# Optimization experiments

Hardware: AMD Instinct MI355X
Metric: run time of the kernel (lower is better)

## Reference

```python
import jax, jax.numpy as jnp
import numpy as np
import math

B, L = 512, 32768
NUM_C, NUM_D = 16, 8
RECIPTIVE, STRIDES = 512, 256
EPS = 1e-4


def setup_inputs() -> dict:
    key = jax.random.key(0)
    kx, kw = jax.random.split(key)
    x = jax.random.normal(kx, (B, L), dtype=jnp.float32)
    stdv = 1.0 / math.sqrt(RECIPTIVE)
    weight = jax.random.uniform(kw, (NUM_C, NUM_D, RECIPTIVE), dtype=jnp.float32,
                                minval=-stdv, maxval=stdv)
    return {"x": x, "weight": weight}


def reference(x, weight):
    # x: [B, L], weight: [C, D, R]
    Lx = x.shape[1]
    # sigma = (W W^T + eps I)^{-1} per capsule, [C, D, D]
    wc = jnp.einsum('cdr,cer->cde', weight, weight)
    sigma = jnp.linalg.inv(wc + EPS * jnp.eye(NUM_D, dtype=weight.dtype))
    # circular sliding windows: [W, R] index map (wraparound matches torch.cat branch)
    starts = jnp.arange(0, Lx, STRIDES)
    idx = (starts[:, None] + jnp.arange(RECIPTIVE)[None, :]) % Lx
    windows = x[:, idx]                                   # [B, W, R]
    proj = jnp.einsum('cdr,bwr->bwcd', weight, windows)    # [B, W, C, D]
    q = jnp.einsum('bwcd,cde,bwce->bwc', proj, sigma, proj)  # quadratic form
    return jnp.mean(jnp.sqrt(q), axis=1)                   # [B, C]
```

## Files before the change

kernel.cpp:

```cpp
#include <hip/hip_runtime.h>
#include <hip/hip_bf16.h>

#define NUM_C  16
#define NUM_D  8
#define RECEPT 512
#define LROW   32768
#define EPS_V  1e-4f

#define XBYTES 33536

typedef __attribute__((ext_vector_type(8))) short short8;
typedef __attribute__((ext_vector_type(4))) float f32x4;

__device__ __forceinline__ unsigned short f2bf(float f) {
    unsigned int u = __builtin_bit_cast(unsigned int, f);
    u += 0x7fffu + ((u >> 16) & 1u);
    return (unsigned short)(u >> 16);
}

__device__ __forceinline__ int xsw(int a) { return a ^ (((a >> 9) & 7) << 4); }

__device__ __forceinline__ ushort4 cvt4(f32x4 v) {
    ushort4 h;
    h.x = f2bf(v[0]); h.y = f2bf(v[1]); h.z = f2bf(v[2]); h.w = f2bf(v[3]);
    return h;
}

__global__ void prep_kernel(const float* __restrict__ weight,
                            unsigned short* __restrict__ wfrag,
                            float* __restrict__ out) {
    __shared__ float Wc[NUM_D * RECEPT];
    __shared__ float G[NUM_D][NUM_D];
    __shared__ float Lm[NUM_D][NUM_D];
    const int c = blockIdx.x;
    const int t = threadIdx.x;

    out[c * 256 + t] = 0.f;
    out[c * 256 + t + 4096] = 0.f;

    const float4* wsrc4 = reinterpret_cast<const float4*>(
        weight + (size_t)c * NUM_D * RECEPT);
    float4* Wc4 = reinterpret_cast<float4*>(Wc);
    #pragma unroll
    for (int i = 0; i < 4; ++i) Wc4[t + i * 256] = wsrc4[t + i * 256];
    __syncthreads();

    if (t < 64) {
        int d = t >> 3, e = t & 7;
        const float4* wd4 = reinterpret_cast<const float4*>(&Wc[d * RECEPT]);
        const float4* we4 = reinterpret_cast<const float4*>(&Wc[e * RECEPT]);
        float s = 0.f;
        #pragma unroll 4
        for (int r4 = 0; r4 < RECEPT / 4; ++r4) {
            float4 a = wd4[r4], bb = we4[r4];
            s += a.x * bb.x + a.y * bb.y + a.z * bb.z + a.w * bb.w;
        }
        if (d == e) s += EPS_V;
        G[d][e] = s;
    }
    __syncthreads();
    if (t == 0) {
        for (int i = 0; i < NUM_D; ++i) {
            float diag = G[i][i];
            for (int k = 0; k < i; ++k) diag -= Lm[i][k] * Lm[i][k];
            float di = sqrtf(diag);
            Lm[i][i] = di;
            float inv = 1.f / di;
            for (int jj = i + 1; jj < NUM_D; ++jj) {
                float s = G[jj][i];
                for (int k = 0; k < i; ++k) s -= Lm[jj][k] * Lm[i][k];
                Lm[jj][i] = s * inv;
            }
        }
    }
    __syncthreads();
    for (int r = t; r < RECEPT; r += 256) {
        float y[NUM_D];
        for (int d = 0; d < NUM_D; ++d) {
            float s = Wc[d * RECEPT + r];
            for (int k = 0; k < d; ++k) s -= Lm[d][k] * y[k];
            y[d] = s / Lm[d][d];
        }
        const int kk = r >> 5;
        const int g  = (r >> 3) & 3;
        const int j  = r & 7;
        for (int d = 0; d < NUM_D; ++d) {
            int cd = c * NUM_D + d;
            int ntile = cd >> 4;
            int nl = cd & 15;
            int lane = g * 16 + nl;
            int idx = (((ntile * 16 + kk) * 64) + lane) * 8 + j;
            wfrag[idx] = f2bf(y[d]);
        }
    }
}

__global__ __launch_bounds__(256, 4) void main_kernel(
        const float* __restrict__ x,
        const unsigned short* __restrict__ wfrag,
        float* __restrict__ out) {
    __shared__ char lds[XBYTES];
    const int bid = blockIdx.x;
    const int b = bid >> 1;
    const int h = bid & 1;
    const int t = threadIdx.x;
    const int lane = t & 63;
    const int wv = t >> 6;
    const int rl = lane & 15;
    const int gl = lane >> 4;
    const int nt0 = wv * 2;

    const char* slice = (const char*)(x + (size_t)b * LROW + h * 16384);

#define XLOAD(dst_, i_) \
    dst_ = __builtin_nontemporal_load( \
        reinterpret_cast<const f32x4*>(slice + ((i_) * 256 + t) * 16))
#define XWRITE(src_, i_) \
    *reinterpret_cast<ushort4*>(lds + xsw(((i_) * 256 + t) * 8)) = cvt4(src_)

    {
        f32x4 p0, p1, p2, p3, q0, q1, q2, q3;
        XLOAD(p0, 0);  XLOAD(p1, 1);  XLOAD(p2, 2);  XLOAD(p3, 3);
        XLOAD(q0, 4);  XLOAD(q1, 5);  XLOAD(q2, 6);  XLOAD(q3, 7);
        XWRITE(p0, 0); XWRITE(p1, 1); XWRITE(p2, 2); XWRITE(p3, 3);
        XLOAD(p0, 8);  XLOAD(p1, 9);  XLOAD(p2, 10); XLOAD(p3, 11);
        XWRITE(q0, 4); XWRITE(q1, 5); XWRITE(q2, 6); XWRITE(q3, 7);
        XLOAD(q0, 12); XLOAD(q1, 13); XLOAD(q2, 14); XLOAD(q3, 15);
        XWRITE(p0, 8); XWRITE(p1, 9); XWRITE(p2, 10); XWRITE(p3, 11);
        XWRITE(q0, 12); XWRITE(q1, 13); XWRITE(q2, 14); XWRITE(q3, 15);
        const char* tsrc = h ? (const char*)(x + (size_t)b * LROW)
                             : slice + 65536;
        if (t < 64) {
            f32x4 vt = __builtin_nontemporal_load(
                reinterpret_cast<const f32x4*>(tsrc + t * 16));
            *reinterpret_cast<ushort4*>(lds + xsw((4096 + t) * 8)) = cvt4(vt);
        }
    }
#undef XLOAD
#undef XWRITE

    f32x4 a00 = {0,0,0,0}, a01 = {0,0,0,0};
    f32x4 a10 = {0,0,0,0}, a11 = {0,0,0,0};
    f32x4 a20 = {0,0,0,0}, a21 = {0,0,0,0};
    f32x4 a30 = {0,0,0,0}, a31 = {0,0,0,0};

    __syncthreads();

    const unsigned short* bptr0 = wfrag + ((size_t)(nt0 * 16) * 64 + lane) * 8;
    const unsigned short* bptr1 = wfrag + ((size_t)((nt0 + 1) * 16) * 64 + lane) * 8;
    const int abase = rl * 512;

    #pragma unroll 2
    for (int kk = 0; kk < 16; ++kk) {
        const int kb = kk * 64 + gl * 16;
        short8 bA = *reinterpret_cast<const short8*>(bptr0);
        short8 bB = *reinterpret_cast<const short8*>(bptr1);
        bptr0 += 512; bptr1 += 512;
        short8 af0 = *reinterpret_cast<const short8*>(lds + xsw(abase + kb));
        short8 af1 = *reinterpret_cast<const short8*>(lds + xsw(abase + 8192 + kb));
        short8 af2 = *reinterpret_cast<const short8*>(lds + xsw(abase + 16384 + kb));
        short8 af3 = *reinterpret_cast<const short8*>(lds + xsw(abase + 24576 + kb));
        a00 = __builtin_amdgcn_mfma_f32_16x16x32_bf16(af0, bA, a00, 0, 0, 0);
        a01 = __builtin_amdgcn_mfma_f32_16x16x32_bf16(af0, bB, a01, 0, 0, 0);
        a10 = __builtin_amdgcn_mfma_f32_16x16x32_bf16(af1, bA, a10, 0, 0, 0);
        a11 = __builtin_amdgcn_mfma_f32_16x16x32_bf16(af1, bB, a11, 0, 0, 0);
        a20 = __builtin_amdgcn_mfma_f32_16x16x32_bf16(af2, bA, a20, 0, 0, 0);
        a21 = __builtin_amdgcn_mfma_f32_16x16x32_bf16(af2, bB, a21, 0, 0, 0);
        a30 = __builtin_amdgcn_mfma_f32_16x16x32_bf16(af3, bA, a30, 0, 0, 0);
        a31 = __builtin_amdgcn_mfma_f32_16x16x32_bf16(af3, bB, a31, 0, 0, 0);
    }

#define SQSUM(s_, A_) { \
    _Pragma("unroll") \
    for (int r = 0; r < 4; ++r) { \
        float p = (A_)[r]; float qq = p * p; \
        qq += __shfl_xor(qq, 1); \
        qq += __shfl_xor(qq, 2); \
        qq += __shfl_xor(qq, 4); \
        s_ += sqrtf(qq); } }

    float s0 = 0.f, s1 = 0.f;
    SQSUM(s0, a00) SQSUM(s0, a10) SQSUM(s0, a20) SQSUM(s0, a30)
    SQSUM(s1, a01) SQSUM(s1, a11) SQSUM(s1, a21) SQSUM(s1, a31)
#undef SQSUM
    s0 += __shfl_xor(s0, 16); s0 += __shfl_xor(s0, 32);
    s1 += __shfl_xor(s1, 16); s1 += __shfl_xor(s1, 32);
    if (lane < 16 && (lane & 7) == 0) {
        int c0 = (wv * 32 + lane) >> 3;
        atomicAdd(&out[b * NUM_C + c0], s0 * (1.0f / 128.0f));
        atomicAdd(&out[b * NUM_C + c0 + 2], s1 * (1.0f / 128.0f));
    }
}

extern "C" void kernel_launch(void* const* d_in, const int* in_sizes, int n_in,
                              void* d_out, int out_size, void* d_ws, size_t ws_size,
                              hipStream_t stream) {
    (void)in_sizes; (void)n_in; (void)ws_size; (void)out_size;
    const float* x      = (const float*)d_in[0];
    const float* weight = (const float*)d_in[1];
    float* out = (float*)d_out;
    unsigned short* wfrag = (unsigned short*)d_ws;

    prep_kernel<<<16, 256, 0, stream>>>(weight, wfrag, out);
    main_kernel<<<1024, 256, 0, stream>>>(x, wfrag, out);
}
```

Measured before the change: 32.48 us.

## Split x staging into two halves and overlap second-half loads with first MFMA pass

Issues all global loads for the slice up front, waits only for the first half with explicit vmcnt, writes it to LDS and runs MFMAs on the first two row groups while the second half is still in flight. The second half, including the wraparound tail, is then written and processed in a second pass. This hides global load latency behind matrix compute. The cost is an extra barrier, weight fragments read twice, more live registers, and hand-written waitcnt counts that depend on the compiler's load ordering.

```diff
diff --git a/kernel.cpp b/kernel.cpp
--- a/kernel.cpp
+++ b/kernel.cpp
@@ -118,57 +118,92 @@
 #define XWRITE(src_, i_) \
     *reinterpret_cast<ushort4*>(lds + xsw(((i_) * 256 + t) * 8)) = cvt4(src_)
 
+    f32x4 L0, L1, L2, L3, L4, L5, L6, L7, M;
+    f32x4 U0, U1, U2, U3, U4, U5, U6, U7, T;
+    XLOAD(L0, 0); XLOAD(L1, 1); XLOAD(L2, 2); XLOAD(L3, 3);
+    XLOAD(L4, 4); XLOAD(L5, 5); XLOAD(L6, 6); XLOAD(L7, 7);
+    if (t < 64)
+        M = __builtin_nontemporal_load(
+            reinterpret_cast<const f32x4*>(slice + (2048 + t) * 16));
+    XLOAD(U0, 8);  XLOAD(U1, 9);  XLOAD(U2, 10); XLOAD(U3, 11);
+    XLOAD(U4, 12); XLOAD(U5, 13); XLOAD(U6, 14); XLOAD(U7, 15);
     {
-        f32x4 p0, p1, p2, p3, q0, q1, q2, q3;
-        XLOAD(p0, 0);  XLOAD(p1, 1);  XLOAD(p2, 2);  XLOAD(p3, 3);
-        XLOAD(q0, 4);  XLOAD(q1, 5);  XLOAD(q2, 6);  XLOAD(q3, 7);
-        XWRITE(p0, 0); XWRITE(p1, 1); XWRITE(p2, 2); XWRITE(p3, 3);
-        XLOAD(p0, 8);  XLOAD(p1, 9);  XLOAD(p2, 10); XLOAD(p3, 11);
-        XWRITE(q0, 4); XWRITE(q1, 5); XWRITE(q2, 6); XWRITE(q3, 7);
-        XLOAD(q0, 12); XLOAD(q1, 13); XLOAD(q2, 14); XLOAD(q3, 15);
-        XWRITE(p0, 8); XWRITE(p1, 9); XWRITE(p2, 10); XWRITE(p3, 11);
-        XWRITE(q0, 12); XWRITE(q1, 13); XWRITE(q2, 14); XWRITE(q3, 15);
         const char* tsrc = h ? (const char*)(x + (size_t)b * LROW)
                              : slice + 65536;
-        if (t < 64) {
-            f32x4 vt = __builtin_nontemporal_load(
+        if (t < 64)
+            T = __builtin_nontemporal_load(
                 reinterpret_cast<const f32x4*>(tsrc + t * 16));
-            *reinterpret_cast<ushort4*>(lds + xsw((4096 + t) * 8)) = cvt4(vt);
-        }
-    }
-#undef XLOAD
-#undef XWRITE
+    }
+
+    if (wv == 0) asm volatile("s_waitcnt vmcnt(9)" ::: "memory");
+    else         asm volatile("s_waitcnt vmcnt(8)" ::: "memory");
+    __builtin_amdgcn_sched_barrier(0);
+
+    XWRITE(L0, 0); XWRITE(L1, 1); XWRITE(L2, 2); XWRITE(L3, 3);
+    XWRITE(L4, 4); XWRITE(L5, 5); XWRITE(L6, 6); XWRITE(L7, 7);
+    if (t < 64)
+        *reinterpret_cast<ushort4*>(lds + xsw((2048 + t) * 8)) = cvt4(M);
 
     f32x4 a00 = {0,0,0,0}, a01 = {0,0,0,0};
     f32x4 a10 = {0,0,0,0}, a11 = {0,0,0,0};
     f32x4 a20 = {0,0,0,0}, a21 = {0,0,0,0};
     f32x4 a30 = {0,0,0,0}, a31 = {0,0,0,0};
 
-    __syncthreads();
-
-    const unsigned short* bptr0 = wfrag + ((size_t)(nt0 * 16) * 64 + lane) * 8;
-    const unsigned short* bptr1 = wfrag + ((size_t)((nt0 + 1) * 16) * 64 + lane) * 8;
-    const int abase = rl * 512;
-
-    #pragma unroll 2
-    for (int kk = 0; kk < 16; ++kk) {
-        const int kb = kk * 64 + gl * 16;
-        short8 bA = *reinterpret_cast<const short8*>(bptr0);
-        short8 bB = *reinterpret_cast<const short8*>(bptr1);
-        bptr0 += 512; bptr1 += 512;
-        short8 af0 = *reinterpret_cast<const short8*>(lds + xsw(abase + kb));
-        short8 af1 = *reinterpret_cast<const short8*>(lds + xsw(abase + 8192 + kb));
-        short8 af2 = *reinterpret_cast<const short8*>(lds + xsw(abase + 16384 + kb));
-        short8 af3 = *reinterpret_cast<const short8*>(lds + xsw(abase + 24576 + kb));
-        a00 = __builtin_amdgcn_mfma_f32_16x16x32_bf16(af0, bA, a00, 0, 0, 0);
-        a01 = __builtin_amdgcn_mfma_f32_16x16x32_bf16(af0, bB, a01, 0, 0, 0);
-        a10 = __builtin_amdgcn_mfma_f32_16x16x32_bf16(af1, bA, a10, 0, 0, 0);
-        a11 = __builtin_amdgcn_mfma_f32_16x16x32_bf16(af1, bB, a11, 0, 0, 0);
-        a20 = __builtin_amdgcn_mfma_f32_16x16x32_bf16(af2, bA, a20, 0, 0, 0);
-        a21 = __builtin_amdgcn_mfma_f32_16x16x32_bf16(af2, bB, a21, 0, 0, 0);
-        a30 = __builtin_amdgcn_mfma_f32_16x16x32_bf16(af3, bA, a30, 0, 0, 0);
-        a31 = __builtin_amdgcn_mfma_f32_16x16x32_bf16(af3, bB, a31, 0, 0, 0);
-    }
+    asm volatile("s_waitcnt lgkmcnt(0)" ::: "memory");
+    __builtin_amdgcn_sched_barrier(0);
+    __builtin_amdgcn_s_barrier();
+    __builtin_amdgcn_sched_barrier(0);
+
+    {
+        const unsigned short* bp0 = wfrag + ((size_t)(nt0 * 16) * 64 + lane) * 8;
+        const unsigned short* bp1 = wfrag + ((size_t)((nt0 + 1) * 16) * 64 + lane) * 8;
+        const int abase = rl * 512;
+        #pragma unroll 2
+        for (int kk = 0; kk < 16; ++kk) {
+            const int kb = kk * 64 + gl * 16;
+            short8 bA = *reinterpret_cast<const short8*>(bp0);
+            short8 bB = *reinterpret_cast<const short8*>(bp1);
+            bp0 += 512; bp1 += 512;
+            short8 af0 = *reinterpret_cast<const short8*>(lds + xsw(abase + kb));
+            short8 af1 = *reinterpret_cast<const short8*>(lds + xsw(abase + 8192 + kb));
+            a00 = __builtin_amdgcn_mfma_f32_16x16x32_bf16(af0, bA, a00, 0, 0, 0);
+            a01 = __builtin_amdgcn_mfma_f32_16x16x32_bf16(af0, bB, a01, 0, 0, 0);
+            a10 = __builtin_amdgcn_mfma_f32_16x16x32_bf16(af1, bA, a10, 0, 0, 0);
+            a11 = __builtin_amdgcn_mfma_f32_16x16x32_bf16(af1, bB, a11, 0, 0, 0);
+        }
+    }
+
+    asm volatile("s_waitcnt vmcnt(0)" ::: "memory");
+    __builtin_amdgcn_sched_barrier(0);
+    XWRITE(U0, 8);  XWRITE(U1, 9);  XWRITE(U2, 10); XWRITE(U3, 11);
+    XWRITE(U4, 12); XWRITE(U5, 13); XWRITE(U6, 14); XWRITE(U7, 15);
+    if (t < 64)
+        *reinterpret_cast<ushort4*>(lds + xsw((4096 + t) * 8)) = cvt4(T);
+    asm volatile("s_waitcnt lgkmcnt(0)" ::: "memory");
+    __builtin_amdgcn_sched_barrier(0);
+    __builtin_amdgcn_s_barrier();
+    __builtin_amdgcn_sched_barrier(0);
+
+    {
+        const unsigned short* bp0 = wfrag + ((size_t)(nt0 * 16) * 64 + lane) * 8;
+        const unsigned short* bp1 = wfrag + ((size_t)((nt0 + 1) * 16) * 64 + lane) * 8;
+        const int abase = rl * 512;
+        #pragma unroll 2
+        for (int kk = 0; kk < 16; ++kk) {
+            const int kb = kk * 64 + gl * 16;
+            short8 bA = *reinterpret_cast<const short8*>(bp0);
+            short8 bB = *reinterpret_cast<const short8*>(bp1);
+            bp0 += 512; bp1 += 512;
+            short8 af2 = *reinterpret_cast<const short8*>(lds + xsw(abase + 16384 + kb));
+            short8 af3 = *reinterpret_cast<const short8*>(lds + xsw(abase + 24576 + kb));
+            a20 = __builtin_amdgcn_mfma_f32_16x16x32_bf16(af2, bA, a20, 0, 0, 0);
+            a21 = __builtin_amdgcn_mfma_f32_16x16x32_bf16(af2, bB, a21, 0, 0, 0);
+            a30 = __builtin_amdgcn_mfma_f32_16x16x32_bf16(af3, bA, a30, 0, 0, 0);
+            a31 = __builtin_amdgcn_mfma_f32_16x16x32_bf16(af3, bB, a31, 0, 0, 0);
+        }
+    }
+#undef XLOAD
+#undef XWRITE
 
 #define SQSUM(s_, A_) { \
     _Pragma("unroll") \
```

After: 35.35 us. 8.8% more time.
